# Kernel tuning notes

Measured on AMD Instinct MI355X. Metric: run time of the kernel, lower is better.

## Reference

```python
import jax, jax.numpy as jnp
import numpy as np
from jax import lax

DN = ('NCHW', 'OIHW', 'NCHW')
KD, VD, C = 32, 128, 256
NCLS, HW_T = 20, 32
LEVEL_SIZES = [128, 64, 32, 16, 8]
BS = 2


def conv2d(x, w, b):
    y = lax.conv_general_dilated(x, w, (1, 1), 'SAME', dimension_numbers=DN)
    return y + b[None, :, None, None]


def resize_bilinear_ac(x, oh, ow):
    # bilinear, align_corners=True, NCHW
    B, Cc, H, W = x.shape
    ys = jnp.linspace(0.0, H - 1.0, oh)
    xs = jnp.linspace(0.0, W - 1.0, ow)
    y0 = jnp.floor(ys).astype(jnp.int32); y1 = jnp.minimum(y0 + 1, H - 1)
    x0 = jnp.floor(xs).astype(jnp.int32); x1 = jnp.minimum(x0 + 1, W - 1)
    wy = (ys - y0).astype(x.dtype); wx = (xs - x0).astype(x.dtype)
    r0 = x[:, :, y0, :]; r1 = x[:, :, y1, :]
    rows = r0 + (r1 - r0) * wy[None, None, :, None]
    c0 = rows[:, :, :, x0]; c1 = rows[:, :, :, x1]
    return c0 + (c1 - c0) * wx[None, None, None, :]


def setup_inputs() -> dict:
    key = jax.random.key(0)
    ks = jax.random.split(key, 16)
    inp = {}
    for i, s in enumerate(LEVEL_SIZES):
        inp[f'feat{i}'] = jax.random.normal(ks[i], (BS, C, s, s), jnp.float32)
    inp['attentions'] = jax.random.normal(ks[5], (NCLS, C, HW_T, HW_T), jnp.float32)
    w = 0.05
    inp['key_t_w'] = jax.random.normal(ks[6], (KD, C, 3, 3), jnp.float32) * w
    inp['key_t_b'] = jax.random.normal(ks[7], (KD,), jnp.float32) * w
    inp['val_t_w'] = jax.random.normal(ks[8], (VD, C, 3, 3), jnp.float32) * w
    inp['val_t_b'] = jax.random.normal(ks[9], (VD,), jnp.float32) * w
    inp['key_q_w'] = jax.random.normal(ks[10], (5, KD, C, 3, 3), jnp.float32) * w
    inp['key_q_b'] = jax.random.normal(ks[11], (5, KD), jnp.float32) * w
    inp['val_q_w'] = jax.random.normal(ks[12], (5, VD, C, 3, 3), jnp.float32) * w
    inp['val_q_b'] = jax.random.normal(ks[13], (5, VD), jnp.float32) * w
    inp['bn_gamma'] = jnp.ones((5, C), jnp.float32)
    inp['bn_beta'] = jnp.zeros((5, C), jnp.float32)
    inp['comb_w'] = jax.random.normal(ks[14], (C, 2 * C, 1, 1), jnp.float32) * w
    inp['comb_b'] = jax.random.normal(ks[15], (C,), jnp.float32) * w
    return inp


def reference(feat0, feat1, feat2, feat3, feat4, attentions,
              key_t_w, key_t_b, val_t_w, val_t_b,
              key_q_w, key_q_b, val_q_w, val_q_b,
              bn_gamma, bn_beta, comb_w, comb_b):
    feats = [feat0, feat1, feat2, feat3, feat4]
    ncls, _, h, w = attentions.shape
    key_t = conv2d(attentions, key_t_w, key_t_b).reshape(ncls, KD, h * w)   # [n,32,t]
    val_t = conv2d(attentions, val_t_w, val_t_b).reshape(ncls, VD, h * w)   # [n,128,t]
    outs = []
    for idx, f in enumerate(feats):
        bs, _, H, W = f.shape
        fc = f - f.mean(axis=(2, 3), keepdims=True)          # subtract foregap
        fr = resize_bilinear_ac(fc, h, w)                    # [b,256,h,w]
        kq = conv2d(fr, key_q_w[idx], key_q_b[idx]).reshape(bs, KD, h * w)  # [b,32,q]
        vq = conv2d(fr, val_q_w[idx], val_q_b[idx]).reshape(bs, VD, h * w)  # [b,128,q]
        # relation: p[b,n,q,t] = kq^T @ key_t ; softmax over q (torch dim=1)
        p = jnp.einsum('bcq,nct->bnqt', kq, key_t)
        p = jax.nn.softmax(p, axis=2)
        # class-summed attended values (sum over n commutes with concat-add loop)
        vt_sum = jnp.einsum('nvq,bnqt->bvt', val_t, p)
        vq_sum = jnp.einsum('bvq,bnqt->bvt', vq, p)
        fin = jnp.concatenate([vq_sum, vt_sum], axis=1).reshape(bs, 2 * VD, h, w)
        fin = resize_bilinear_ac(fin, H, W)
        # BatchNorm2d (training-mode batch stats, eps=1e-5)
        mu = fin.mean(axis=(0, 2, 3), keepdims=True)
        var = fin.var(axis=(0, 2, 3), keepdims=True)
        fin = (fin - mu) * lax.rsqrt(var + 1e-5)
        fin = fin * bn_gamma[idx][None, :, None, None] + bn_beta[idx][None, :, None, None]
        out = conv2d(jnp.concatenate([f, fin], axis=1), comb_w, comb_b)
        outs.append(out)
    return tuple(outs)
```

## Files before the change

### kernel.cpp

```cpp
#include <hip/hip_runtime.h>
#include <cstddef>
#include <cstdint>

typedef __attribute__((ext_vector_type(8))) short bf16x8;
typedef __attribute__((ext_vector_type(16))) float f32x16;
typedef __attribute__((ext_vector_type(4))) unsigned short us4;

static const size_t B_BIASC = 0;
static const size_t B_KTH   = 3840;
static const size_t B_KTL   = 1314560;
static const size_t B_VT    = 2625280;
static const size_t B_KQH   = 7868160;
static const size_t B_KQL   = 8523520;
static const size_t B_VQ    = 9178880;
static const size_t B_MEAN  = 11800320;
static const size_t B_FSM   = 11810560;
static const size_t B_MU    = 17053440;
static const size_t B_VAR   = 17058560;
static const size_t B_WC    = 17063680;
static const size_t B_BIAS2 = 18374400;
static const size_t B_UNION = 18379520;
static const size_t U_XH    = 0;
static const size_t U_XL    = 15728640;
static const size_t U_WPH   = 31457280;
static const size_t U_WPL   = 35880960;
static const size_t U_FPART = 0;
static const size_t B_ML    = 60322560;
static const size_t WS_BYTES = 60977920;

__device__ inline unsigned short f2bf(float x) {
    unsigned u = __float_as_uint(x);
    return (unsigned short)((u + 0x7fffu + ((u >> 16) & 1u)) >> 16);
}
__device__ inline float bf2f(unsigned short u) {
    return __uint_as_float(((unsigned)u) << 16);
}
__device__ inline void bf16split(float x, unsigned short& hi, unsigned short& lo) {
    unsigned u = __float_as_uint(x);
    unsigned hb = (u + 0x7fffu + ((u >> 16) & 1u)) >> 16;
    hi = (unsigned short)hb;
    float hf = __uint_as_float(hb << 16);
    float r = x - hf;
    unsigned ur = __float_as_uint(r);
    lo = (unsigned short)((ur + 0x7fffu + ((ur >> 16) & 1u)) >> 16);
}
__device__ inline const float* sel5(const float* a, const float* b, const float* c,
                                    const float* d, const float* e, int i) {
    return i == 0 ? a : i == 1 ? b : i == 2 ? c : i == 3 ? d : e;
}

__global__ __launch_bounds__(256) void prep_weights(
    const float* __restrict__ kt_w, const float* __restrict__ kt_b,
    const float* __restrict__ vt_w, const float* __restrict__ vt_b,
    const float* __restrict__ kq_w, const float* __restrict__ kq_b,
    const float* __restrict__ vq_w, const float* __restrict__ vq_b,
    short* __restrict__ wp_hi, short* __restrict__ wp_lo, float* __restrict__ biasc)
{
    const int oc = blockIdx.x;
    const int s  = blockIdx.y;
    const int ic = threadIdx.x;
    const bool iskey = oc < 32;
    const int ocl = iskey ? oc : oc - 32;
    const float scale = (iskey && s > 0) ? 1.4426950408889634f : 1.0f;
    const float* w = iskey
        ? (s == 0 ? kt_w : kq_w + (size_t)(s - 1) * 32 * 256 * 9)
        : (s == 0 ? vt_w : vq_w + (size_t)(s - 1) * 128 * 256 * 9);
    const float* wsrc = w + ((size_t)ocl * 256 + ic) * 9;
#pragma unroll
    for (int t = 0; t < 9; ++t) {
        unsigned short h, l; bf16split(wsrc[t] * scale, h, l);
        size_t d = ((size_t)(s * 9 + t) * 160 + oc) * 256 + ic;
        wp_hi[d] = (short)h; wp_lo[d] = (short)l;
    }
    if (ic == 0) {
        const float* bptr = iskey
            ? (s == 0 ? kt_b : kq_b + (s - 1) * 32)
            : (s == 0 ? vt_b : vq_b + (s - 1) * 128);
        biasc[s * 160 + oc] = bptr[ocl] * scale;
    }
}

__global__ __launch_bounds__(256) void transpose_split(
    const float* __restrict__ in,
    unsigned short* __restrict__ oh, unsigned short* __restrict__ ol)
{
    __shared__ float s[16][260];
    const int n = blockIdx.x, ch = blockIdx.y, p0 = blockIdx.z * 256;
    const int tid = threadIdx.x;
#pragma unroll
    for (int i = 0; i < 16; ++i)
        s[i][tid] = in[((size_t)(n * 256 + ch * 16 + i)) * 1024 + p0 + tid];
    __syncthreads();
    union { unsigned short u[16]; bf16x8 v[2]; } h8, l8;
#pragma unroll
    for (int i = 0; i < 16; ++i) bf16split(s[i][tid], h8.u[i], l8.u[i]);
    size_t base = ((size_t)(n * 16 + ch) * 1024 + p0 + tid) * 16;
    *(bf16x8*)&oh[base] = h8.v[0]; *(bf16x8*)&oh[base + 8] = h8.v[1];
    *(bf16x8*)&ol[base] = l8.v[0]; *(bf16x8*)&ol[base + 8] = l8.v[1];
}

__global__ __launch_bounds__(256) void mean2d_all(
    const float* f0, const float* f1, const float* f2, const float* f3, const float* f4,
    float* __restrict__ mean)
{
    const int lvl = blockIdx.y;
    const float* f = sel5(f0, f1, f2, f3, f4, lvl);
    const int H = 128 >> lvl, HW = H * H;
    const int bc = blockIdx.x;
    const float* src = f + (size_t)bc * HW;
    float s = 0.f;
    for (int i = threadIdx.x; i < HW; i += 256) s += src[i];
#pragma unroll
    for (int off = 32; off; off >>= 1) s += __shfl_xor(s, off);
    __shared__ float red[4];
    if ((threadIdx.x & 63) == 0) red[threadIdx.x >> 6] = s;
    __syncthreads();
    if (threadIdx.x == 0)
        mean[lvl * 512 + bc] = (red[0] + red[1] + red[2] + red[3]) / (float)HW;
}

__global__ __launch_bounds__(256) void resizeT_all(
    const float* f0, const float* f1, const float* f2, const float* f3, const float* f4,
    const float* __restrict__ mean,
    unsigned short* __restrict__ oh, unsigned short* __restrict__ ol)
{
    __shared__ float s[16][260];
    const int lvl = blockIdx.z >> 2;
    const int p0 = (blockIdx.z & 3) * 256;
    const int b = blockIdx.x, ch = blockIdx.y;
    const float* f = sel5(f0, f1, f2, f3, f4, lvl);
    const int H = 128 >> lvl;
    const int img = 20 + lvl * 2 + b;
    const int tid = threadIdx.x;
    const int p = p0 + tid, y = p >> 5, x = p & 31;
    float fy = (float)y * (float)(H - 1) / 31.0f;
    float fx = (float)x * (float)(H - 1) / 31.0f;
    int y0 = (int)fy; int y1 = min(y0 + 1, H - 1); float wy = fy - (float)y0;
    int x0 = (int)fx; int x1 = min(x0 + 1, H - 1); float wx = fx - (float)x0;
#pragma unroll
    for (int i = 0; i < 16; ++i) {
        int c = ch * 16 + i;
        const float* pf = f + ((size_t)(b * 256 + c)) * H * H;
        float a = pf[y0 * H + x0], bb = pf[y1 * H + x0];
        float cc = pf[y0 * H + x1], d = pf[y1 * H + x1];
        float c0 = a + (bb - a) * wy;
        float c1 = cc + (d - cc) * wy;
        s[i][tid] = c0 + (c1 - c0) * wx - mean[lvl * 512 + b * 256 + c];
    }
    __syncthreads();
    union { unsigned short u[16]; bf16x8 v[2]; } h8, l8;
#pragma unroll
    for (int i = 0; i < 16; ++i) bf16split(s[i][tid], h8.u[i], l8.u[i]);
    size_t base = ((size_t)(img * 16 + ch) * 1024 + p) * 16;
    *(bf16x8*)&oh[base] = h8.v[0]; *(bf16x8*)&oh[base + 8] = h8.v[1];
    *(bf16x8*)&ol[base] = l8.v[0]; *(bf16x8*)&ol[base + 8] = l8.v[1];
}

__global__ __launch_bounds__(256) void conv3x3_all(
    const unsigned short* __restrict__ xT_h,
    const unsigned short* __restrict__ xT_l,
    const short* __restrict__ wp_hi_all,
    const short* __restrict__ wp_lo_all,
    const float* __restrict__ biasc_all,
    unsigned short* __restrict__ kt_hi, unsigned short* __restrict__ kt_lo,
    unsigned short* __restrict__ vt,
    unsigned short* __restrict__ kq_hi, unsigned short* __restrict__ kq_lo,
    unsigned short* __restrict__ vq)
{
    const int bid = blockIdx.x;
    const int xcd = bid & 7;
    const int j   = bid >> 3;
    const int grp = j % 5;
    const int k   = j / 5;
    const int yp  = k & 15;
    const int imgh = k >> 4;
    const int img = xcd + 8 * imgh;
    if (img >= 30) return;

    __shared__ float s_red[4][2][16][64];
    const int tid = threadIdx.x;
    const bool iskey = (grp == 0);
    const int set = (img < 20) ? 0 : 1 + ((img - 20) >> 1);
    const int ocb = grp * 32;
    const int wave = tid >> 6, lane = tid & 63, l31 = tid & 31, lh = (tid >> 5) & 1;
    const int y0 = yp * 2;

    f32x16 acc0 = {}, acc1 = {};
    const bf16x8 bz = {};
    const unsigned short* xh = xT_h + (size_t)img * 16 * 16384;
    const unsigned short* xl = xT_l + (size_t)img * 16 * 16384;
    const short* wph = wp_hi_all + (size_t)set * 368640;
    const short* wpl = wp_lo_all + (size_t)set * 368640;
    const float* bset = biasc_all + set * 160;

    for (int cc = 0; cc < 4; ++cc) {
        const int ch = (wave << 2) + cc;
        const unsigned short* xhc = xh + (size_t)ch * 16384 + lh * 8;
        const unsigned short* xlc = xl + (size_t)ch * 16384 + lh * 8;
#pragma unroll
        for (int tg = 0; tg < 3; ++tg) {
            bf16x8 wh[3], wl[3];
#pragma unroll
            for (int tl = 0; tl < 3; ++tl) {
                size_t wi = ((size_t)((tg * 3 + tl) * 160 + ocb + l31)) * 256 + (ch << 4) + lh * 8;
                wh[tl] = *(const bf16x8*)&wph[wi];
                if (iskey) wl[tl] = *(const bf16x8*)&wpl[wi];
            }
#pragma unroll
            for (int nt = 0; nt < 2; ++nt) {
                const int ri = y0 + nt - 1 + tg;
                const bool rok = (ri >= 0 && ri < 32);
#pragma unroll
                for (int tl = 0; tl < 3; ++tl) {
                    const int x = l31 + tl - 1;
                    const bool ok = rok && (x >= 0) && (x < 32);
                    bf16x8 bh = bz, bl = bz;
                    if (ok) {
                        const int p = ri * 32 + x;
                        bh = *(const bf16x8*)&xhc[p * 16];
                        if (iskey) bl = *(const bf16x8*)&xlc[p * 16];
                    }
                    f32x16& a = nt ? acc1 : acc0;
                    a = __builtin_amdgcn_mfma_f32_32x32x16_bf16(wh[tl], bh, a, 0, 0, 0);
                    if (iskey) {
                        a = __builtin_amdgcn_mfma_f32_32x32x16_bf16(wh[tl], bl, a, 0, 0, 0);
                        a = __builtin_amdgcn_mfma_f32_32x32x16_bf16(wl[tl], bh, a, 0, 0, 0);
                    }
                }
            }
        }
    }
#pragma unroll
    for (int r = 0; r < 16; ++r) {
        s_red[wave][0][r][lane] = acc0[r];
        s_red[wave][1][r][lane] = acc1[r];
    }
    __syncthreads();
    float r0[4], r1[4];
#pragma unroll
    for (int jj = 0; jj < 4; ++jj) {
        int r = (wave << 2) + jj;
        r0[jj] = s_red[0][0][r][lane] + s_red[1][0][r][lane] + s_red[2][0][r][lane] + s_red[3][0][r][lane];
        r1[jj] = s_red[0][1][r][lane] + s_red[1][1][r][lane] + s_red[2][1][r][lane] + s_red[3][1][r][lane];
    }
    if (iskey) {
#pragma unroll
        for (int nt = 0; nt < 2; ++nt) {
            const float* rr = nt ? r1 : r0;
            int p = (y0 + nt) * 32 + l31;
            int ocq = 8 * wave + 4 * lh;
            us4 h4, l4;
#pragma unroll
            for (int jj = 0; jj < 4; ++jj) {
                unsigned short h, l;
                bf16split(rr[jj] + bset[ocq + jj], h, l);
                h4[jj] = h; l4[jj] = l;
            }
            if (img < 20) {
                size_t base = ((size_t)img * 1024 + p) * 32;
                *(us4*)&kt_hi[base + ocq] = h4;
                *(us4*)&kt_lo[base + ocq] = l4;
            } else {
                size_t base = ((size_t)(img - 20) * 1024 + p) * 32;
                *(us4*)&kq_hi[base + ocq] = h4;
                *(us4*)&kq_lo[base + ocq] = l4;
            }
        }
    } else {
#pragma unroll
        for (int nt = 0; nt < 2; ++nt) {
            const float* rr = nt ? r1 : r0;
            int p = (y0 + nt) * 32 + l31;
#pragma unroll
            for (int jj = 0; jj < 4; ++jj) {
                int pat = jj + 8 * wave + 4 * lh;
                int vo = (ocb - 32) + pat;
                unsigned short val = f2bf(rr[jj] + bset[32 + vo]);
                if (img < 20) vt[((size_t)img * 128 + vo) * 1024 + p] = val;
                else          vq[((size_t)(img - 20) * 128 + vo) * 1024 + p] = val;
            }
        }
    }
}

__global__ __launch_bounds__(256, 2) void flash5(
    const unsigned short* __restrict__ kt_hi, const unsigned short* __restrict__ kt_lo,
    const unsigned short* __restrict__ vt_bf,
    const unsigned short* __restrict__ kq_hi, const unsigned short* __restrict__ kq_lo,
    const unsigned short* __restrict__ vq_bf,
    unsigned short* __restrict__ part2,
    float2* __restrict__ ml_out)
{
    const int tid = threadIdx.x;
    const int t0 = blockIdx.x * 64;
    const int b  = blockIdx.y;
    const int n  = blockIdx.z >> 1;
    const int qg = blockIdx.z & 1;
    const int qbase = qg * 512;
    const int wave = tid >> 6, lane = tid & 63, l31 = lane & 31, lh = lane >> 5;
    const int tw = wave & 1, vw = wave >> 1;

    const int trow = t0 + tw * 32 + l31;
    bf16x8 btk_h0, btk_h1, btk_l0, btk_l1;
    {
        size_t g = ((size_t)n * 1024 + trow) * 32 + lh * 8;
        btk_h0 = *(const bf16x8*)&kt_hi[g];
        btk_h1 = *(const bf16x8*)&kt_hi[g + 16];
        btk_l0 = *(const bf16x8*)&kt_lo[g];
        btk_l1 = *(const bf16x8*)&kt_lo[g + 16];
    }

    const unsigned short* vbase = (vw == 0)
        ? (vq_bf + (size_t)b * 131072)
        : (vt_bf + (size_t)n * 131072);
    const unsigned short* vrow[4];
#pragma unroll
    for (int vs = 0; vs < 4; ++vs)
        vrow[vs] = vbase + ((size_t)(vs * 32 + l31)) * 1024 + lh * 8;

    const unsigned short* kqh = kq_hi + (size_t)b * 1024 * 32;
    const unsigned short* kql = kq_lo + (size_t)b * 1024 * 32;

    bf16x8 nva[4][2];
#pragma unroll
    for (int vs = 0; vs < 4; ++vs) {
        nva[vs][0] = *(const bf16x8*)&vrow[vs][qbase];
        nva[vs][1] = *(const bf16x8*)&vrow[vs][qbase + 16];
    }
    bf16x8 nah0 = *(const bf16x8*)&kqh[(size_t)(qbase + l31) * 32 + lh * 8];
    bf16x8 nah1 = *(const bf16x8*)&kqh[(size_t)(qbase + l31) * 32 + 16 + lh * 8];
    bf16x8 nal0 = *(const bf16x8*)&kql[(size_t)(qbase + l31) * 32 + lh * 8];
    bf16x8 nal1 = *(const bf16x8*)&kql[(size_t)(qbase + l31) * 32 + 16 + lh * 8];

    f32x16 acc0 = {}, acc1 = {}, acc2 = {}, acc3 = {};
    float m = -3.0e38f, lsum = 0.f;

    for (int q0 = qbase; q0 < qbase + 512; q0 += 32) {
        bf16x8 va[4][2];
#pragma unroll
        for (int vs = 0; vs < 4; ++vs) { va[vs][0] = nva[vs][0]; va[vs][1] = nva[vs][1]; }
        bf16x8 ah0 = nah0, ah1 = nah1, al0 = nal0, al1 = nal1;

        if (q0 + 32 < qbase + 512) {
            const int qn = q0 + 32;
#pragma unroll
            for (int vs = 0; vs < 4; ++vs) {
                nva[vs][0] = *(const bf16x8*)&vrow[vs][qn];
                nva[vs][1] = *(const bf16x8*)&vrow[vs][qn + 16];
            }
            size_t kb = (size_t)(qn + l31) * 32 + lh * 8;
            nah0 = *(const bf16x8*)&kqh[kb];
            nah1 = *(const bf16x8*)&kqh[kb + 16];
            nal0 = *(const bf16x8*)&kql[kb];
            nal1 = *(const bf16x8*)&kql[kb + 16];
        }

        f32x16 s = {};
        __builtin_amdgcn_s_setprio(1);
        s = __builtin_amdgcn_mfma_f32_32x32x16_bf16(ah0, btk_h0, s, 0, 0, 0);
        s = __builtin_amdgcn_mfma_f32_32x32x16_bf16(ah0, btk_l0, s, 0, 0, 0);
        s = __builtin_amdgcn_mfma_f32_32x32x16_bf16(al0, btk_h0, s, 0, 0, 0);
        s = __builtin_amdgcn_mfma_f32_32x32x16_bf16(ah1, btk_h1, s, 0, 0, 0);
        s = __builtin_amdgcn_mfma_f32_32x32x16_bf16(ah1, btk_l1, s, 0, 0, 0);
        s = __builtin_amdgcn_mfma_f32_32x32x16_bf16(al1, btk_h1, s, 0, 0, 0);
        __builtin_amdgcn_s_setprio(0);

        float pmax = s[0];
#pragma unroll
        for (int r = 1; r < 16; ++r) pmax = fmaxf(pmax, s[r]);
        pmax = fmaxf(pmax, __shfl_xor(pmax, 32));
        if (!__all(pmax <= m + 11.5417f)) {
            float mnew = fmaxf(m, pmax);
            float sc = __builtin_amdgcn_exp2f(m - mnew);
            m = mnew; lsum *= sc;
            acc0 *= sc; acc1 *= sc; acc2 *= sc; acc3 *= sc;
        }
        float pv[16]; float ps = 0.f;
#pragma unroll
        for (int r = 0; r < 16; ++r) { pv[r] = __builtin_amdgcn_exp2f(s[r] - m); ps += pv[r]; }
        lsum += ps;

        unsigned a0, a1, a2, a3, c0, c1, c2, c3;
        asm("v_cvt_pk_bf16_f32 %0, %1, %2" : "=v"(a0) : "v"(pv[0]),  "v"(pv[1]));
        asm("v_cvt_pk_bf16_f32 %0, %1, %2" : "=v"(a1) : "v"(pv[2]),  "v"(pv[3]));
        asm("v_cvt_pk_bf16_f32 %0, %1, %2" : "=v"(a2) : "v"(pv[4]),  "v"(pv[5]));
        asm("v_cvt_pk_bf16_f32 %0, %1, %2" : "=v"(a3) : "v"(pv[6]),  "v"(pv[7]));
        asm("v_cvt_pk_bf16_f32 %0, %1, %2" : "=v"(c0) : "v"(pv[8]),  "v"(pv[9]));
        asm("v_cvt_pk_bf16_f32 %0, %1, %2" : "=v"(c1) : "v"(pv[10]), "v"(pv[11]));
        asm("v_cvt_pk_bf16_f32 %0, %1, %2" : "=v"(c2) : "v"(pv[12]), "v"(pv[13]));
        asm("v_cvt_pk_bf16_f32 %0, %1, %2" : "=v"(c3) : "v"(pv[14]), "v"(pv[15]));
        asm("v_permlane32_swap_b32 %0, %1" : "+v"(a0), "+v"(a2));
        asm("v_permlane32_swap_b32 %0, %1" : "+v"(a1), "+v"(a3));
        asm("v_permlane32_swap_b32 %0, %1" : "+v"(c0), "+v"(c2));
        asm("v_permlane32_swap_b32 %0, %1" : "+v"(c1), "+v"(c3));
        union { unsigned u[4]; bf16x8 v; } f0, f1;
        f0.u[0] = a0; f0.u[1] = a1; f0.u[2] = a2; f0.u[3] = a3;
        f1.u[0] = c0; f1.u[1] = c1; f1.u[2] = c2; f1.u[3] = c3;

        __builtin_amdgcn_s_setprio(1);
#pragma unroll
        for (int vs = 0; vs < 4; ++vs) {
            f32x16& a = (vs == 0) ? acc0 : (vs == 1) ? acc1 : (vs == 2) ? acc2 : acc3;
            a = __builtin_amdgcn_mfma_f32_32x32x16_bf16(va[vs][0], f0.v, a, 0, 0, 0);
            a = __builtin_amdgcn_mfma_f32_32x32x16_bf16(va[vs][1], f1.v, a, 0, 0, 0);
        }
        __builtin_amdgcn_s_setprio(0);
    }

    float lt = lsum + __shfl_xor(lsum, 32);
    float linv = 1.f / lt;
    const int tg = t0 + tw * 32 + l31;
    const size_t slab = (size_t)((qg * 20 + n) * 2 + b);
    unsigned short* outp = part2 + slab * 262144;
#pragma unroll
    for (int vs = 0; vs < 4; ++vs) {
        const f32x16& a = (vs == 0) ? acc0 : (vs == 1) ? acc1 : (vs == 2) ? acc2 : acc3;
#pragma unroll
        for (int r = 0; r < 16; ++r) {
            int v = vw * 128 + vs * 32 + (r & 3) + 8 * (r >> 2) + 4 * lh;
            outp[(size_t)v * 1024 + tg] = f2bf(a[r] * linv);
        }
    }
    if (vw == 0 && lh == 0)
        ml_out[slab * 1024 + tg] = make_float2(m, lt);
}

__global__ __launch_bounds__(256) void reduce40_merge(
    const unsigned short* __restrict__ part,
    const float2* __restrict__ ml,
    unsigned short* __restrict__ out)
{
    size_t i = (size_t)blockIdx.x * 256 + threadIdx.x;
    const int t = (int)(i & 1023);
    const int b = (int)(i >> 18);
    const int vt_off = (int)(i & 262143);
    float s = 0.f;
#pragma unroll
    for (int n = 0; n < 20; ++n) {
        float2 ml0 = ml[(size_t)((0 * 20 + n) * 2 + b) * 1024 + t];
        float2 ml1 = ml[(size_t)((20 + n) * 2 + b) * 1024 + t];
        float M = fmaxf(ml0.x, ml1.x);
        float w0 = ml0.y * __builtin_amdgcn_exp2f(ml0.x - M);
        float w1 = ml1.y * __builtin_amdgcn_exp2f(ml1.x - M);
        float inv = 1.f / (w0 + w1);
        float v0 = bf2f(part[(size_t)((0 * 20 + n) * 2 + b) * 262144 + vt_off]);
        float v1 = bf2f(part[(size_t)((20 + n) * 2 + b) * 262144 + vt_off]);
        s += (v0 * w0 + v1 * w1) * inv;
    }
    out[i] = f2bf(s);
}

__global__ __launch_bounds__(256) void bnstats2_all(
    const unsigned short* __restrict__ fsm, float* __restrict__ mu, float* __restrict__ var)
{
    const int c = blockIdx.x, lvl = blockIdx.y;
    const int lg = 7 - lvl, H = 128 >> lvl, HW = H * H;
    const float sc = 31.f / (float)(H - 1);
    float s = 0.f, s2 = 0.f;
    for (int u = threadIdx.x; u < 2 * HW; u += 256) {
        int b = (u >= HW) ? 1 : 0;
        int p = u - b * HW;
        int y = p >> lg, x = p & (H - 1);
        float fy = (float)y * sc, fx = (float)x * sc;
        int y0 = (int)fy, x0 = (int)fx;
        int y1 = min(y0 + 1, 31), x1 = min(x0 + 1, 31);
        float wy = fy - (float)y0, wx = fx - (float)x0;
        const unsigned short* src = fsm + ((size_t)(lvl * 2 + b) * 256 + c) * 1024;
        float a = bf2f(src[y0 * 32 + x0]), bb = bf2f(src[y1 * 32 + x0]);
        float cc = bf2f(src[y0 * 32 + x1]), d = bf2f(src[y1 * 32 + x1]);
        float c0 = a + (bb - a) * wy;
        float c1 = cc + (d - cc) * wy;
        float v = c0 + (c1 - c0) * wx;
        s += v; s2 += v * v;
    }
#pragma unroll
    for (int off = 32; off; off >>= 1) {
        s  += __shfl_xor(s, off);
        s2 += __shfl_xor(s2, off);
    }
    __shared__ float r1[4], r2[4];
    if ((threadIdx.x & 63) == 0) { r1[threadIdx.x >> 6] = s; r2[threadIdx.x >> 6] = s2; }
    __syncthreads();
    if (threadIdx.x == 0) {
        float cnt = 2.f * (float)HW;
        float mm = (r1[0] + r1[1] + r1[2] + r1[3]) / cnt;
        float qq = (r2[0] + r2[1] + r2[2] + r2[3]) / cnt;
        mu[lvl * 256 + c] = mm; var[lvl * 256 + c] = qq - mm * mm;
    }
}

__global__ __launch_bounds__(256) void prep_comb_all(
    const float* __restrict__ comb_w, const float* __restrict__ comb_b,
    const float* __restrict__ gamma, const float* __restrict__ beta,
    const float* __restrict__ mu, const float* __restrict__ var,
    short* __restrict__ wc, float* __restrict__ bias2)
{
    const int oc = blockIdx.x, lvl = blockIdx.y;
    const int ic = threadIdx.x;
    float a  = gamma[lvl * 256 + ic] * rsqrtf(var[lvl * 256 + ic] + 1e-5f);
    float bb = beta[lvl * 256 + ic] - mu[lvl * 256 + ic] * a;
    float w1 = comb_w[(size_t)oc * 512 + ic];
    float w2 = comb_w[(size_t)oc * 512 + 256 + ic];
    short* wcl = wc + (size_t)lvl * 131072;
    wcl[(size_t)oc * 512 + ic]       = (short)f2bf(w1);
    wcl[(size_t)oc * 512 + 256 + ic] = (short)f2bf(w2 * a);
    float s = w2 * bb;
#pragma unroll
    for (int off = 32; off; off >>= 1) s += __shfl_xor(s, off);
    __shared__ float red[4];
    if ((threadIdx.x & 63) == 0) red[threadIdx.x >> 6] = s;
    __syncthreads();
    if (threadIdx.x == 0)
        bias2[lvl * 256 + oc] = comb_b[oc] + red[0] + red[1] + red[2] + red[3];
}

__global__ __launch_bounds__(256, 1) void comb_all(
    const float* f0, const float* f1, const float* f2, const float* f3, const float* f4,
    const unsigned short* __restrict__ fsm,
    const short* __restrict__ wc_all,
    const float* __restrict__ bias2_all,
    float* __restrict__ out)
{
    __shared__ short s_wc[256 * 40];
    __shared__ short s_xc[128 * 40];
    const int bx = blockIdx.x;
    int lvl, x0;
    if      (bx < 128) { lvl = 0; x0 = bx; }
    else if (bx < 160) { lvl = 1; x0 = bx - 128; }
    else if (bx < 168) { lvl = 2; x0 = bx - 160; }
    else if (bx < 170) { lvl = 3; x0 = bx - 168; }
    else               { lvl = 4; x0 = bx - 170; }
    const int H = 128 >> lvl, HW = H * H;
    const int lg = 7 - lvl, Hm = H - 1;
    const float scl = 31.f / (float)Hm;
    static const size_t CUM[5] = {0, 8388608, 10485760, 11010048, 11141120};
    const float* f = sel5(f0, f1, f2, f3, f4, lvl);
    const short* wc = wc_all + (size_t)lvl * 131072;
    const float* bias2 = bias2_all + lvl * 256;
    float* outl = out + CUM[lvl];

    const int tid = threadIdx.x;
    const int p0 = x0 * 128;
    const int b  = blockIdx.y;
    const int wv = tid >> 6, l31 = tid & 31, lh = (tid >> 5) & 1;
    const int wm = wv >> 1, wn = wv & 1;

    f32x16 acc[4][2];
#pragma unroll
    for (int i = 0; i < 4; ++i)
#pragma unroll
        for (int j = 0; j < 2; ++j)
#pragma unroll
            for (int r = 0; r < 16; ++r) acc[i][j][r] = 0.f;

    for (int k0 = 0; k0 < 512; k0 += 32) {
        __syncthreads();
        for (int u = tid; u < 512; u += 256) {
            int r = u >> 1, h = u & 1;
            *(bf16x8*)&s_wc[r * 40 + h * 16 + 0] = *(const bf16x8*)&wc[(size_t)r * 512 + k0 + h * 16];
            *(bf16x8*)&s_wc[r * 40 + h * 16 + 8] = *(const bf16x8*)&wc[(size_t)r * 512 + k0 + h * 16 + 8];
        }
        for (int u = tid; u < 1024; u += 256) {
            int kr = u >> 5, n4 = (u & 31) * 4;
            int ck = k0 + kr;
            if (ck < 256) {
                const float* bsrc = f + ((size_t)(b * 256 + ck)) * HW;
                int p = p0 + n4;
                float v0, v1, v2, v3;
                if (p + 3 < HW) {
                    float4 v4 = *(const float4*)&bsrc[p];
                    v0 = v4.x; v1 = v4.y; v2 = v4.z; v3 = v4.w;
                } else {
                    v0 = bsrc[min(p,     HW - 1)];
                    v1 = bsrc[min(p + 1, HW - 1)];
                    v2 = bsrc[min(p + 2, HW - 1)];
                    v3 = bsrc[min(p + 3, HW - 1)];
                }
                s_xc[(n4 + 0) * 40 + kr] = (short)f2bf(v0);
                s_xc[(n4 + 1) * 40 + kr] = (short)f2bf(v1);
                s_xc[(n4 + 2) * 40 + kr] = (short)f2bf(v2);
                s_xc[(n4 + 3) * 40 + kr] = (short)f2bf(v3);
            } else {
                int c = ck - 256;
                const unsigned short* src = fsm + ((size_t)(lvl * 2 + b) * 256 + c) * 1024;
#pragma unroll
                for (int j = 0; j < 4; ++j) {
                    int pp = min(p0 + n4 + j, HW - 1);
                    int y = pp >> lg, x = pp & Hm;
                    float fy = (float)y * scl, fx = (float)x * scl;
                    int y0 = (int)fy, x0i = (int)fx;
                    int y1 = min(y0 + 1, 31), x1 = min(x0i + 1, 31);
                    float wy = fy - (float)y0, wx = fx - (float)x0i;
                    float a = bf2f(src[y0 * 32 + x0i]), bb = bf2f(src[y1 * 32 + x0i]);
                    float cc = bf2f(src[y0 * 32 + x1]), d = bf2f(src[y1 * 32 + x1]);
                    float c0 = a + (bb - a) * wy;
                    float c1 = cc + (d - cc) * wy;
                    s_xc[(n4 + j) * 40 + kr] = (short)f2bf(c0 + (c1 - c0) * wx);
                }
            }
        }
        __syncthreads();
#pragma unroll
        for (int ks = 0; ks < 2; ++ks) {
            bf16x8 a[4], bx2[2];
#pragma unroll
            for (int mi = 0; mi < 4; ++mi)
                a[mi] = *(const bf16x8*)&s_wc[(wm * 128 + mi * 32 + l31) * 40 + ks * 16 + lh * 8];
#pragma unroll
            for (int ni = 0; ni < 2; ++ni)
                bx2[ni] = *(const bf16x8*)&s_xc[(wn * 64 + ni * 32 + l31) * 40 + ks * 16 + lh * 8];
#pragma unroll
            for (int mi = 0; mi < 4; ++mi)
#pragma unroll
                for (int ni = 0; ni < 2; ++ni)
                    acc[mi][ni] = __builtin_amdgcn_mfma_f32_32x32x16_bf16(a[mi], bx2[ni], acc[mi][ni], 0, 0, 0);
        }
    }
#pragma unroll
    for (int mi = 0; mi < 4; ++mi) {
#pragma unroll
        for (int ni = 0; ni < 2; ++ni) {
            int p = p0 + wn * 64 + ni * 32 + l31;
            if (p < HW) {
#pragma unroll
                for (int r = 0; r < 16; ++r) {
                    int oc = wm * 128 + mi * 32 + (r & 3) + 8 * (r >> 2) + 4 * lh;
                    outl[((size_t)(b * 256 + oc)) * HW + p] = acc[mi][ni][r] + bias2[oc];
                }
            }
        }
    }
}

extern "C" void kernel_launch(void* const* d_in, const int* in_sizes, int n_in,
                              void* d_out, int out_size, void* d_ws, size_t ws_size,
                              hipStream_t stream) {
    if (ws_size < WS_BYTES) return;

    const float* feats[5];
    for (int i = 0; i < 5; ++i) feats[i] = (const float*)d_in[i];
    const float* attn     = (const float*)d_in[5];
    const float* key_t_w  = (const float*)d_in[6];
    const float* key_t_b  = (const float*)d_in[7];
    const float* val_t_w  = (const float*)d_in[8];
    const float* val_t_b  = (const float*)d_in[9];
    const float* key_q_w  = (const float*)d_in[10];
    const float* key_q_b  = (const float*)d_in[11];
    const float* val_q_w  = (const float*)d_in[12];
    const float* val_q_b  = (const float*)d_in[13];
    const float* bn_gamma = (const float*)d_in[14];
    const float* bn_beta  = (const float*)d_in[15];
    const float* comb_w   = (const float*)d_in[16];
    const float* comb_b   = (const float*)d_in[17];

    char* ws = (char*)d_ws;
    float* biasc = (float*)(ws + B_BIASC);
    unsigned short* kt_hi = (unsigned short*)(ws + B_KTH);
    unsigned short* kt_lo = (unsigned short*)(ws + B_KTL);
    unsigned short* vt    = (unsigned short*)(ws + B_VT);
    unsigned short* kq_hi = (unsigned short*)(ws + B_KQH);
    unsigned short* kq_lo = (unsigned short*)(ws + B_KQL);
    unsigned short* vq    = (unsigned short*)(ws + B_VQ);
    float* mean_f = (float*)(ws + B_MEAN);
    unsigned short* fsm = (unsigned short*)(ws + B_FSM);
    float* mu     = (float*)(ws + B_MU);
    float* var    = (float*)(ws + B_VAR);
    short* wc_bf  = (short*)(ws + B_WC);
    float* bias2  = (float*)(ws + B_BIAS2);
    unsigned short* X_h = (unsigned short*)(ws + B_UNION + U_XH);
    unsigned short* X_l = (unsigned short*)(ws + B_UNION + U_XL);
    short* wp_hi = (short*)(ws + B_UNION + U_WPH);
    short* wp_lo = (short*)(ws + B_UNION + U_WPL);
    unsigned short* part2 = (unsigned short*)(ws + B_UNION + U_FPART);
    float2* ml_arr = (float2*)(ws + B_ML);

    prep_weights<<<dim3(160, 6), 256, 0, stream>>>(
        key_t_w, key_t_b, val_t_w, val_t_b, key_q_w, key_q_b, val_q_w, val_q_b,
        wp_hi, wp_lo, biasc);

    transpose_split<<<dim3(20, 16, 4), 256, 0, stream>>>(attn, X_h, X_l);

    mean2d_all<<<dim3(512, 5), 256, 0, stream>>>(
        feats[0], feats[1], feats[2], feats[3], feats[4], mean_f);

    resizeT_all<<<dim3(2, 16, 20), 256, 0, stream>>>(
        feats[0], feats[1], feats[2], feats[3], feats[4], mean_f, X_h, X_l);

    conv3x3_all<<<2560, 256, 0, stream>>>(
        X_h, X_l, wp_hi, wp_lo, biasc, kt_hi, kt_lo, vt, kq_hi, kq_lo, vq);

    for (int idx = 0; idx < 5; ++idx) {
        flash5<<<dim3(16, 2, 40), 256, 0, stream>>>(
            kt_hi, kt_lo, vt,
            kq_hi + (size_t)idx * 2 * 32768,
            kq_lo + (size_t)idx * 2 * 32768,
            vq + (size_t)idx * 2 * 131072,
            part2, ml_arr);

        reduce40_merge<<<2048, 256, 0, stream>>>(part2, ml_arr, fsm + (size_t)idx * 524288);
    }

    bnstats2_all<<<dim3(256, 5), 256, 0, stream>>>(fsm, mu, var);

    prep_comb_all<<<dim3(256, 5), 256, 0, stream>>>(
        comb_w, comb_b, bn_gamma, bn_beta, mu, var, wc_bf, bias2);

    comb_all<<<dim3(171, 2), 256, 0, stream>>>(
        feats[0], feats[1], feats[2], feats[3], feats[4],
        fsm, wc_bf, bias2, (float*)d_out);
}
```

Before: 871.1 us.

## Split flash into single-wave blocks, precompute upsampled features, shrink comb tiles

The flash attention kernel now launches one 64-thread wave per block, covering 32 targets and one value half, instead of four waves per block. This gives the scheduler more, smaller blocks. A new upsample_all kernel materialises the bilinear-upsampled attention features in bf16 once, so comb_all no longer recomputes the 4-tap interpolation inside its GEMM staging loop. comb_all uses 64-pixel tiles with a 2x2 MFMA accumulator per wave, doubling the grid for better occupancy. The trade-off is an extra kernel launch plus a round trip through global memory for the upsampled tensor, and lower per-block data reuse.

```diff
diff --git a/kernel.cpp b/kernel.cpp
--- a/kernel.cpp
+++ b/kernel.cpp
@@ -283,7 +283,7 @@
     }
 }
 
-__global__ __launch_bounds__(256, 2) void flash5(
+__global__ __launch_bounds__(64, 4) void flash6(
     const unsigned short* __restrict__ kt_hi, const unsigned short* __restrict__ kt_lo,
     const unsigned short* __restrict__ vt_bf,
     const unsigned short* __restrict__ kq_hi, const unsigned short* __restrict__ kq_lo,
@@ -292,15 +292,15 @@
     float2* __restrict__ ml_out)
 {
     const int tid = threadIdx.x;
-    const int t0 = blockIdx.x * 64;
-    const int b  = blockIdx.y;
-    const int n  = blockIdx.z >> 1;
-    const int qg = blockIdx.z & 1;
+    const int l31 = tid & 31, lh = tid >> 5;
+    const int t32 = blockIdx.x >> 1;
+    const int vw  = blockIdx.x & 1;
+    const int b   = blockIdx.y;
+    const int n   = blockIdx.z >> 1;
+    const int qg  = blockIdx.z & 1;
     const int qbase = qg * 512;
-    const int wave = tid >> 6, lane = tid & 63, l31 = lane & 31, lh = lane >> 5;
-    const int tw = wave & 1, vw = wave >> 1;
-
-    const int trow = t0 + tw * 32 + l31;
+
+    const int trow = t32 * 32 + l31;
     bf16x8 btk_h0, btk_h1, btk_l0, btk_l1;
     {
         size_t g = ((size_t)n * 1024 + trow) * 32 + lh * 8;
@@ -409,7 +409,6 @@
 
     float lt = lsum + __shfl_xor(lsum, 32);
     float linv = 1.f / lt;
-    const int tg = t0 + tw * 32 + l31;
     const size_t slab = (size_t)((qg * 20 + n) * 2 + b);
     unsigned short* outp = part2 + slab * 262144;
 #pragma unroll
@@ -418,11 +417,11 @@
 #pragma unroll
         for (int r = 0; r < 16; ++r) {
             int v = vw * 128 + vs * 32 + (r & 3) + 8 * (r >> 2) + 4 * lh;
-            outp[(size_t)v * 1024 + tg] = f2bf(a[r] * linv);
+            outp[(size_t)v * 1024 + trow] = f2bf(a[r] * linv);
         }
     }
     if (vw == 0 && lh == 0)
-        ml_out[slab * 1024 + tg] = make_float2(m, lt);
+        ml_out[slab * 1024 + trow] = make_float2(m, lt);
 }
 
 __global__ __launch_bounds__(256) void reduce40_merge(
@@ -448,6 +447,35 @@
         s += (v0 * w0 + v1 * w1) * inv;
     }
     out[i] = f2bf(s);
+}
+
+__global__ __launch_bounds__(256) void upsample_all(
+    const unsigned short* __restrict__ fsm, unsigned short* __restrict__ finup)
+{
+    static const size_t CUMF[5] = {0, 8388608, 10485760, 11010048, 11141120};
+    const int lvl = blockIdx.y;
+    const int lg = 7 - lvl, H = 128 >> lvl, HW = H * H;
+    int idx = blockIdx.x * 256 + threadIdx.x;
+    if (idx >= (2 * 256 * HW) >> 2) return;
+    const int p4 = (idx << 2) & (HW - 1);
+    const int bc = (idx << 2) >> (2 * lg);
+    const int y = p4 >> lg, x = p4 & (H - 1);
+    const float sc = 31.f / (float)(H - 1);
+    float fy = (float)y * sc;
+    int y0 = (int)fy; int y1 = min(y0 + 1, 31); float wy = fy - (float)y0;
+    const unsigned short* src = fsm + ((size_t)(lvl * 512 + bc)) * 1024;
+    us4 o;
+#pragma unroll
+    for (int j = 0; j < 4; ++j) {
+        float fx = (float)(x + j) * sc;
+        int x0 = (int)fx; int x1 = min(x0 + 1, 31); float wx = fx - (float)x0;
+        float a = bf2f(src[y0 * 32 + x0]), bb = bf2f(src[y1 * 32 + x0]);
+        float cc = bf2f(src[y0 * 32 + x1]), d = bf2f(src[y1 * 32 + x1]);
+        float c0 = a + (bb - a) * wy;
+        float c1 = cc + (d - cc) * wy;
+        o[j] = f2bf(c0 + (c1 - c0) * wx);
+    }
+    *(us4*)&finup[CUMF[lvl] + (size_t)bc * HW + p4] = o;
 }
 
 __global__ __launch_bounds__(256) void bnstats2_all(
@@ -516,38 +544,36 @@
 
 __global__ __launch_bounds__(256, 1) void comb_all(
     const float* f0, const float* f1, const float* f2, const float* f3, const float* f4,
-    const unsigned short* __restrict__ fsm,
+    const unsigned short* __restrict__ finup,
     const short* __restrict__ wc_all,
     const float* __restrict__ bias2_all,
     float* __restrict__ out)
 {
     __shared__ short s_wc[256 * 40];
-    __shared__ short s_xc[128 * 40];
+    __shared__ short s_xc[64 * 40];
+    static const size_t CUM[5] = {0, 8388608, 10485760, 11010048, 11141120};
     const int bx = blockIdx.x;
     int lvl, x0;
-    if      (bx < 128) { lvl = 0; x0 = bx; }
-    else if (bx < 160) { lvl = 1; x0 = bx - 128; }
-    else if (bx < 168) { lvl = 2; x0 = bx - 160; }
-    else if (bx < 170) { lvl = 3; x0 = bx - 168; }
-    else               { lvl = 4; x0 = bx - 170; }
+    if      (bx < 256) { lvl = 0; x0 = bx; }
+    else if (bx < 320) { lvl = 1; x0 = bx - 256; }
+    else if (bx < 336) { lvl = 2; x0 = bx - 320; }
+    else if (bx < 340) { lvl = 3; x0 = bx - 336; }
+    else               { lvl = 4; x0 = 0; }
     const int H = 128 >> lvl, HW = H * H;
-    const int lg = 7 - lvl, Hm = H - 1;
-    const float scl = 31.f / (float)Hm;
-    static const size_t CUM[5] = {0, 8388608, 10485760, 11010048, 11141120};
     const float* f = sel5(f0, f1, f2, f3, f4, lvl);
+    const unsigned short* fup = finup + CUM[lvl];
     const short* wc = wc_all + (size_t)lvl * 131072;
     const float* bias2 = bias2_all + lvl * 256;
     float* outl = out + CUM[lvl];
 
     const int tid = threadIdx.x;
-    const int p0 = x0 * 128;
+    const int p0 = x0 * 64;
     const int b  = blockIdx.y;
     const int wv = tid >> 6, l31 = tid & 31, lh = (tid >> 5) & 1;
-    const int wm = wv >> 1, wn = wv & 1;
-
-    f32x16 acc[4][2];
-#pragma unroll
-    for (int i = 0; i < 4; ++i)
+
+    f32x16 acc[2][2];
+#pragma unroll
+    for (int i = 0; i < 2; ++i)
 #pragma unroll
         for (int j = 0; j < 2; ++j)
 #pragma unroll
@@ -560,73 +586,50 @@
             *(bf16x8*)&s_wc[r * 40 + h * 16 + 0] = *(const bf16x8*)&wc[(size_t)r * 512 + k0 + h * 16];
             *(bf16x8*)&s_wc[r * 40 + h * 16 + 8] = *(const bf16x8*)&wc[(size_t)r * 512 + k0 + h * 16 + 8];
         }
-        for (int u = tid; u < 1024; u += 256) {
-            int kr = u >> 5, n4 = (u & 31) * 4;
+        for (int u = tid; u < 512; u += 256) {
+            int kr = u >> 4, n4 = (u & 15) * 4;
             int ck = k0 + kr;
+            int p = p0 + n4;
             if (ck < 256) {
-                const float* bsrc = f + ((size_t)(b * 256 + ck)) * HW;
-                int p = p0 + n4;
-                float v0, v1, v2, v3;
-                if (p + 3 < HW) {
-                    float4 v4 = *(const float4*)&bsrc[p];
-                    v0 = v4.x; v1 = v4.y; v2 = v4.z; v3 = v4.w;
-                } else {
-                    v0 = bsrc[min(p,     HW - 1)];
-                    v1 = bsrc[min(p + 1, HW - 1)];
-                    v2 = bsrc[min(p + 2, HW - 1)];
-                    v3 = bsrc[min(p + 3, HW - 1)];
-                }
-                s_xc[(n4 + 0) * 40 + kr] = (short)f2bf(v0);
-                s_xc[(n4 + 1) * 40 + kr] = (short)f2bf(v1);
-                s_xc[(n4 + 2) * 40 + kr] = (short)f2bf(v2);
-                s_xc[(n4 + 3) * 40 + kr] = (short)f2bf(v3);
+                float4 v4 = *(const float4*)&f[((size_t)(b * 256 + ck)) * HW + p];
+                s_xc[(n4 + 0) * 40 + kr] = (short)f2bf(v4.x);
+                s_xc[(n4 + 1) * 40 + kr] = (short)f2bf(v4.y);
+                s_xc[(n4 + 2) * 40 + kr] = (short)f2bf(v4.z);
+                s_xc[(n4 + 3) * 40 + kr] = (short)f2bf(v4.w);
             } else {
-                int c = ck - 256;
-                const unsigned short* src = fsm + ((size_t)(lvl * 2 + b) * 256 + c) * 1024;
-#pragma unroll
-                for (int j = 0; j < 4; ++j) {
-                    int pp = min(p0 + n4 + j, HW - 1);
-                    int y = pp >> lg, x = pp & Hm;
-                    float fy = (float)y * scl, fx = (float)x * scl;
-                    int y0 = (int)fy, x0i = (int)fx;
-                    int y1 = min(y0 + 1, 31), x1 = min(x0i + 1, 31);
-                    float wy = fy - (float)y0, wx = fx - (float)x0i;
-                    float a = bf2f(src[y0 * 32 + x0i]), bb = bf2f(src[y1 * 32 + x0i]);
-                    float cc = bf2f(src[y0 * 32 + x1]), d = bf2f(src[y1 * 32 + x1]);
-                    float c0 = a + (bb - a) * wy;
-                    float c1 = cc + (d - cc) * wy;
-                    s_xc[(n4 + j) * 40 + kr] = (short)f2bf(c0 + (c1 - c0) * wx);
-                }
+                us4 v4 = *(const us4*)&fup[((size_t)(b * 256 + ck - 256)) * HW + p];
+                s_xc[(n4 + 0) * 40 + kr] = (short)v4[0];
+                s_xc[(n4 + 1) * 40 + kr] = (short)v4[1];
+                s_xc[(n4 + 2) * 40 + kr] = (short)v4[2];
+                s_xc[(n4 + 3) * 40 + kr] = (short)v4[3];
             }
         }
         __syncthreads();
 #pragma unroll
         for (int ks = 0; ks < 2; ++ks) {
-            bf16x8 a[4], bx2[2];
-#pragma unroll
-            for (int mi = 0; mi < 4; ++mi)
-                a[mi] = *(const bf16x8*)&s_wc[(wm * 128 + mi * 32 + l31) * 40 + ks * 16 + lh * 8];
+            bf16x8 a[2], bx2[2];
+#pragma unroll
+            for (int mi = 0; mi < 2; ++mi)
+                a[mi] = *(const bf16x8*)&s_wc[(wv * 64 + mi * 32 + l31) * 40 + ks * 16 + lh * 8];
 #pragma unroll
             for (int ni = 0; ni < 2; ++ni)
-                bx2[ni] = *(const bf16x8*)&s_xc[(wn * 64 + ni * 32 + l31) * 40 + ks * 16 + lh * 8];
-#pragma unroll
-            for (int mi = 0; mi < 4; ++mi)
+                bx2[ni] = *(const bf16x8*)&s_xc[(ni * 32 + l31) * 40 + ks * 16 + lh * 8];
+#pragma unroll
+            for (int mi = 0; mi < 2; ++mi)
 #pragma unroll
                 for (int ni = 0; ni < 2; ++ni)
                     acc[mi][ni] = __builtin_amdgcn_mfma_f32_32x32x16_bf16(a[mi], bx2[ni], acc[mi][ni], 0, 0, 0);
         }
     }
 #pragma unroll
-    for (int mi = 0; mi < 4; ++mi) {
+    for (int mi = 0; mi < 2; ++mi) {
 #pragma unroll
         for (int ni = 0; ni < 2; ++ni) {
-            int p = p0 + wn * 64 + ni * 32 + l31;
-            if (p < HW) {
-#pragma unroll
-                for (int r = 0; r < 16; ++r) {
-                    int oc = wm * 128 + mi * 32 + (r & 3) + 8 * (r >> 2) + 4 * lh;
-                    outl[((size_t)(b * 256 + oc)) * HW + p] = acc[mi][ni][r] + bias2[oc];
-                }
+            int p = p0 + ni * 32 + l31;
+#pragma unroll
+            for (int r = 0; r < 16; ++r) {
+                int oc = wv * 64 + mi * 32 + (r & 3) + 8 * (r >> 2) + 4 * lh;
+                outl[((size_t)(b * 256 + oc)) * HW + p] = acc[mi][ni][r] + bias2[oc];
             }
         }
     }
@@ -673,6 +676,7 @@
     short* wp_lo = (short*)(ws + B_UNION + U_WPL);
     unsigned short* part2 = (unsigned short*)(ws + B_UNION + U_FPART);
     float2* ml_arr = (float2*)(ws + B_ML);
+    unsigned short* finup = (unsigned short*)(ws + B_UNION);
 
     prep_weights<<<dim3(160, 6), 256, 0, stream>>>(
         key_t_w, key_t_b, val_t_w, val_t_b, key_q_w, key_q_b, val_q_w, val_q_b,
@@ -690,7 +694,7 @@
         X_h, X_l, wp_hi, wp_lo, biasc, kt_hi, kt_lo, vt, kq_hi, kq_lo, vq);
 
     for (int idx = 0; idx < 5; ++idx) {
-        flash5<<<dim3(16, 2, 40), 256, 0, stream>>>(
+        flash6<<<dim3(64, 2, 40), 64, 0, stream>>>(
             kt_hi, kt_lo, vt,
             kq_hi + (size_t)idx * 2 * 32768,
             kq_lo + (size_t)idx * 2 * 32768,
@@ -700,12 +704,14 @@
         reduce40_merge<<<2048, 256, 0, stream>>>(part2, ml_arr, fsm + (size_t)idx * 524288);
     }
 
+    upsample_all<<<dim3(8192, 5), 256, 0, stream>>>(fsm, finup);
+
     bnstats2_all<<<dim3(256, 5), 256, 0, stream>>>(fsm, mu, var);
 
     prep_comb_all<<<dim3(256, 5), 256, 0, stream>>>(
         comb_w, comb_b, bn_gamma, bn_beta, mu, var, wc_bf, bias2);
 
-    comb_all<<<dim3(171, 2), 256, 0, stream>>>(
+    comb_all<<<dim3(341, 2), 256, 0, stream>>>(
         feats[0], feats[1], feats[2], feats[3], feats[4],
-        fsm, wc_bf, bias2, (float*)d_out);
-}
+        finup, wc_bf, bias2, (float*)d_out);
+}
```

Measured after the change: 2.562 ms. 194% more time.
